# Optimization experiments

Hardware: AMD Instinct MI355X
Metric: run time of the kernel (lower is better)

## Reference

```python
import jax, jax.numpy as jnp
import numpy as np

N_NODES = 131072
N_EDGES = 2097152
B = 256
NODES_PER_GRAPH = 512  # uniform graphs -> to_dense_batch == reshape
F_IN = 74
D = 128
L = 3
EPS = 1e-5


def setup_inputs() -> dict:
    key = jax.random.key(0)
    ks = jax.random.split(key, 12)
    x = jax.random.normal(ks[0], (N_NODES, F_IN), dtype=jnp.float32)
    edge_index = jax.random.randint(ks[1], (2, N_EDGES), 0, N_NODES, dtype=jnp.int32)
    batch = (jnp.arange(N_NODES, dtype=jnp.int32) // NODES_PER_GRAPH)
    s = 1.0 / np.sqrt(D)
    W_init = jax.random.uniform(ks[2], (F_IN, D), jnp.float32, -s, s)
    W_gcn = jax.random.uniform(ks[3], (L, D, D), jnp.float32, -s, s)
    b_gcn = jnp.zeros((L, D), jnp.float32)
    gamma = jnp.ones((L, D), jnp.float32)
    beta = jnp.zeros((L, D), jnp.float32)
    W_res = jax.random.uniform(ks[4], (L, D, D), jnp.float32, -s, s)
    b_res = jax.random.uniform(ks[5], (L, D), jnp.float32, -s, s)
    return {"x": x, "edge_index": edge_index, "batch": batch, "W_init": W_init,
            "W_gcn": W_gcn, "b_gcn": b_gcn, "gamma": gamma, "beta": beta,
            "W_res": W_res, "b_res": b_res}


def _gcn_conv(x, src, tgt, norm, W, b):
    # PyG GCNConv: h = x @ W ; out[tgt] += norm * h[src] ; + bias
    h = x @ W                                    # [N, D]
    msg = h[src] * norm[:, None]                 # [E+N, D] gather (memory-bound)
    out = jax.ops.segment_sum(msg, tgt, num_segments=N_NODES)
    return out + b


def _batchnorm(x, g, bta):
    mean = jnp.mean(x, axis=0)
    var = jnp.var(x, axis=0)  # biased, matches torch BN training forward
    return (x - mean) * jax.lax.rsqrt(var + EPS) * g + bta


def reference(x, edge_index, batch, W_init, W_gcn, b_gcn, gamma, beta, W_res, b_res):
    # add self loops once; symmetric deg^{-1/2} normalization (PyG default)
    loops = jnp.arange(N_NODES, dtype=edge_index.dtype)
    src = jnp.concatenate([edge_index[0], loops])
    tgt = jnp.concatenate([edge_index[1], loops])
    deg = jax.ops.segment_sum(jnp.ones_like(src, dtype=jnp.float32), tgt,
                              num_segments=N_NODES)
    dinv = jnp.where(deg > 0, jax.lax.rsqrt(jnp.maximum(deg, 1.0)), 0.0)
    norm = dinv[src] * dinv[tgt]

    h = x @ W_init                               # init_transform (no bias)
    for i in range(L):
        conv = _gcn_conv(h, src, tgt, norm, W_gcn[i], b_gcn[i])
        h_new = jax.nn.relu(_batchnorm(conv, gamma[i], beta[i]))
        h = h_new + (h @ W_res[i] + b_res[i])
    # to_dense_batch with uniform NODES_PER_GRAPH -> reshape, all mask=True
    return h.reshape(B, NODES_PER_GRAPH, D)
```

## Files before the change

kernel.cpp:

```cpp
#include <hip/hip_runtime.h>

#define NN 131072
#define NE 2097152
#define DD 128
#define LL 3

#define NB 256
#define BSH 9
#define TILE (NE / NB)

typedef __attribute__((ext_vector_type(8))) short short8;
typedef __attribute__((ext_vector_type(4))) float f32x4;

__device__ __forceinline__ ushort f2bf(float f) {
    uint u = __float_as_uint(f);
    return (ushort)((u + 0x7fffu + ((u >> 16) & 1u)) >> 16);
}
__device__ __forceinline__ float bflo(uint u) { return __uint_as_float(u << 16); }
__device__ __forceinline__ float bfhi(uint u) { return __uint_as_float(u & 0xffff0000u); }

__global__ __launch_bounds__(256) void k_prep(const float* __restrict__ x,
                                              const float* __restrict__ Wi,
                                              const float* __restrict__ Wg,
                                              const float* __restrict__ Wr,
                                              uint* __restrict__ xb,
                                              ushort* __restrict__ wt,
                                              float* __restrict__ bns) {
    const int t = threadIdx.x, blk = blockIdx.x;
    const size_t id = (size_t)blk * 256 + t;
    const int n = (int)(id >> 6);
    const int k0 = (int)(id & 63) * 2;
    float v0 = (k0 < 74) ? x[(size_t)n * 74 + k0] : 0.0f;
    float v1 = (k0 + 1 < 74) ? x[(size_t)n * 74 + k0 + 1] : 0.0f;
    xb[id] = (uint)f2bf(v0) | ((uint)f2bf(v1) << 16);
    if (blk < 448) {
        const int id2 = blk * 256 + t;
        const int m = id2 >> 14;
        const int c = (id2 >> 7) & 127;
        const int k = id2 & 127;
        float v;
        if (m == 0)      v = (k < 74) ? Wi[k * DD + c] : 0.0f;
        else if (m <= 3) v = Wg[(size_t)(m - 1) * DD * DD + k * DD + c];
        else             v = Wr[(size_t)(m - 4) * DD * DD + k * DD + c];
        wt[id2] = f2bf(v);
    }
    if (blk == 448) {
        bns[t] = 0.0f; bns[t + 256] = 0.0f; bns[t + 512] = 0.0f;
    }
}

__global__ __launch_bounds__(256) void kA_count(const int* __restrict__ tgt,
                                                int* __restrict__ blockHist) {
    __shared__ int hist[NB];
    const int t = threadIdx.x, blk = blockIdx.x;
    hist[t] = 0;
    __syncthreads();
    const int base = blk * TILE;
#pragma unroll 8
    for (int j = 0; j < TILE / 256; ++j)
        atomicAdd(&hist[tgt[base + j * 256 + t] >> BSH], 1);
    __syncthreads();
    blockHist[t * NB + blk] = hist[t];
}

__global__ __launch_bounds__(256) void kA_scan1(int* __restrict__ blockHist,
                                                int* __restrict__ rowSum) {
    __shared__ int sc[256];
    const int t = threadIdx.x, b = blockIdx.x;
    const int v = blockHist[b * NB + t];
    sc[t] = v;
    __syncthreads();
    for (int off = 1; off < 256; off <<= 1) {
        int a = sc[t];
        int u = (t >= off) ? sc[t - off] : 0;
        __syncthreads();
        sc[t] = a + u;
        __syncthreads();
    }
    blockHist[b * NB + t] = sc[t] - v;
    if (t == 255) rowSum[b] = sc[255];
}

__global__ __launch_bounds__(256) void kA_scan2(const int* __restrict__ rowSum,
                                                int* __restrict__ bstart) {
    __shared__ int sc[256];
    const int t = threadIdx.x;
    const int v = rowSum[t];
    sc[t] = v;
    __syncthreads();
    for (int off = 1; off < 256; off <<= 1) {
        int a = sc[t];
        int u = (t >= off) ? sc[t - off] : 0;
        __syncthreads();
        sc[t] = a + u;
        __syncthreads();
    }
    bstart[t] = sc[t] - v;
    if (t == 255) bstart[NB] = sc[255];
}

__global__ __launch_bounds__(256) void kA_scatter(const int* __restrict__ src,
                                                  const int* __restrict__ tgt,
                                                  const int* __restrict__ chunkBase,
                                                  const int* __restrict__ bstart,
                                                  uint* __restrict__ packed) {
    __shared__ int cur[NB];
    const int t = threadIdx.x, blk = blockIdx.x;
    cur[t] = bstart[t] + chunkBase[t * NB + blk];
    __syncthreads();
    const int base = blk * TILE;
#pragma unroll 4
    for (int j = 0; j < TILE / 256; ++j) {
        const int e = base + j * 256 + t;
        const int tg = tgt[e], s = src[e];
        const int b = tg >> BSH;
        const int pos = atomicAdd(&cur[b], 1);
        packed[pos] = (uint)s | ((uint)(tg & ((1 << BSH) - 1)) << 17);
    }
}

__global__ __launch_bounds__(256) void kB_sort(const uint* __restrict__ packed,
                                               const int* __restrict__ bstart,
                                               int* __restrict__ rowp,
                                               float* __restrict__ dinv,
                                               int* __restrict__ deg,
                                               int* __restrict__ ssrc) {
    __shared__ int cnt[1 << BSH];
    __shared__ int pscan[256];
    const int t = threadIdx.x, b = blockIdx.x;
    const int e0 = bstart[b], e1 = bstart[b + 1];
    cnt[t] = 0; cnt[t + 256] = 0;
    __syncthreads();
    for (int e = e0 + t; e < e1; e += 256)
        atomicAdd(&cnt[packed[e] >> 17], 1);
    __syncthreads();
    const int c0 = cnt[2 * t], c1 = cnt[2 * t + 1];
    pscan[t] = c0 + c1;
    __syncthreads();
    for (int off = 1; off < 256; off <<= 1) {
        int v = pscan[t];
        int u = (t >= off) ? pscan[t - off] : 0;
        __syncthreads();
        pscan[t] = v + u;
        __syncthreads();
    }
    const int ex0 = pscan[t] - c0 - c1;
    const int ex1 = ex0 + c0;
    const int n0 = (b << BSH) + 2 * t;
    rowp[n0] = e0 + ex0;
    rowp[n0 + 1] = e0 + ex1;
    dinv[n0] = rsqrtf((float)(c0 + 1));
    dinv[n0 + 1] = rsqrtf((float)(c1 + 1));
    deg[n0] = c0 + 1;
    deg[n0 + 1] = c1 + 1;
    if (b == NB - 1 && t == 255) rowp[NN] = e1;
    __syncthreads();
    cnt[2 * t] = ex0;
    cnt[2 * t + 1] = ex1;
    __syncthreads();
    for (int e = e0 + t; e < e1; e += 256) {
        const uint p = packed[e];
        const int tl = p >> 17;
        const int pos = atomicAdd(&cnt[tl], 1);
        ssrc[e0 + pos] = (int)(p & 0x1FFFFu);
    }
}

__global__ __launch_bounds__(256) void k_pack(int* __restrict__ ssrc,
                                              const int* __restrict__ deg) {
    const int e = blockIdx.x * 256 + threadIdx.x;
    const int s = ssrc[e];
    ssrc[e] = s | (deg[s] << 17);
}

template <int MODE>
__global__ __launch_bounds__(512) void k_mgemm(const ushort* A,
                                               const ushort* __restrict__ Bt,
                                               ushort* outb,
                                               float* __restrict__ outf,
                                               const ushort* __restrict__ convb,
                                               const float* __restrict__ gamma,
                                               const float* __restrict__ beta,
                                               const float* __restrict__ bres,
                                               float* __restrict__ bnsums) {
    __shared__ ushort As[16384];
    __shared__ ushort Bs[16384];
    __shared__ float sred[256];
    const int t = threadIdx.x;
    const int w = t >> 6, l = t & 63;
    const int lc = l & 15, lr = l >> 4;
    const size_t row0 = (size_t)blockIdx.x * 128;

    for (int ch = w * 4; ch < w * 4 + 4; ++ch) {
        const int row = ch * 4 + lr;
        const int kb = (lc * 16) ^ ((row & 7) << 4);
        const ushort* srcA = A + (row0 + row) * DD + (kb >> 1);
        const ushort* srcB = Bt + (size_t)row * DD + (kb >> 1);
        __builtin_amdgcn_global_load_lds(
            (const __attribute__((address_space(1))) void*)srcA,
            (__attribute__((address_space(3))) void*)(As + ch * 512), 16, 0, 0);
        __builtin_amdgcn_global_load_lds(
            (const __attribute__((address_space(1))) void*)srcB,
            (__attribute__((address_space(3))) void*)(Bs + ch * 512), 16, 0, 0);
    }
    if (MODE == 1 && t < 256) sred[t] = 0.0f;
    if (MODE >= 2 && t < DD) {
        const float invN = 1.0f / (float)NN;
        const float mean = bnsums[t] * invN;
        const float var = bnsums[DD + t] * invN - mean * mean;
        const float sc = gamma[t] * rsqrtf(var + 1e-5f);
        sred[t] = sc;
        sred[DD + t] = beta[t] - mean * sc;
    }
    __syncthreads();

    f32x4 acc[8] = {};
    const char* Ab = (const char*)As;
    const char* Bb = (const char*)Bs;
#pragma unroll
    for (int kk = 0; kk < 4; ++kk) {
        const int kb = kk * 64 + lr * 16;
        const int r = w * 16 + lc;
        const short8 a = *(const short8*)(Ab + r * 256 + (kb ^ ((r & 7) << 4)));
#pragma unroll
        for (int n = 0; n < 8; ++n) {
            const int c = n * 16 + lc;
            short8 b = *(const short8*)(Bb + c * 256 + (kb ^ ((c & 7) << 4)));
            acc[n] = __builtin_amdgcn_mfma_f32_16x16x32_bf16(a, b, acc[n], 0, 0, 0);
        }
    }

    if (MODE == 0) {
#pragma unroll
        for (int n = 0; n < 8; ++n) {
            const int c = n * 16 + lc;
#pragma unroll
            for (int j = 0; j < 4; ++j) {
                const size_t r = row0 + w * 16 + lr * 4 + j;
                outb[r * DD + c] = f2bf(acc[n][j]);
            }
        }
    } else if (MODE == 1) {
#pragma unroll
        for (int n = 0; n < 8; ++n) {
            const int c = n * 16 + lc;
            float ps = 0.0f, ps2 = 0.0f;
#pragma unroll
            for (int j = 0; j < 4; ++j) {
                const size_t r = row0 + w * 16 + lr * 4 + j;
                const float v = acc[n][j];
                outb[r * DD + c] = f2bf(v);
                ps += v; ps2 += v * v;
            }
            atomicAdd(&sred[c], ps);
            atomicAdd(&sred[DD + c], ps2);
        }
        __syncthreads();
        if (t < 256) atomicAdd(&bnsums[t], sred[t]);
    } else {
        float scv[8], shv[8], bbv[8];
#pragma unroll
        for (int n = 0; n < 8; ++n) {
            const int c = n * 16 + lc;
            scv[n] = sred[c]; shv[n] = sred[DD + c]; bbv[n] = bres[c];
        }
#pragma unroll
        for (int n = 0; n < 8; ++n) {
            const int c = n * 16 + lc;
#pragma unroll
            for (int j = 0; j < 4; ++j) {
                const size_t r = row0 + w * 16 + lr * 4 + j;
                const float cv = __uint_as_float((uint)convb[r * DD + c] << 16);
                const float v = fmaxf(cv * scv[n] + shv[n], 0.0f) + acc[n][j] + bbv[n];
                if (MODE == 2) outb[r * DD + c] = f2bf(v);
                if (MODE == 3) outf[r * DD + c] = v;
            }
        }
    }
}

__global__ __launch_bounds__(256) void k_aggregate(const int* __restrict__ rowp,
                                                   const float* __restrict__ dinv,
                                                   const int* __restrict__ ssrc,
                                                   const uint* __restrict__ hb,
                                                   uint* __restrict__ aggb) {
    __shared__ float2 eb[4][64];
    const int wv = threadIdx.x >> 6;
    const int n = blockIdx.x * 4 + wv;
    const int l = threadIdx.x & 63;
    const float dn = dinv[n];
    const uint u0 = hb[((uint)n << 6) + l];
    const float dn2 = dn * dn;
    float ax = dn2 * bflo(u0), ay = dn2 * bfhi(u0);
    const int e0 = rowp[n], e1 = rowp[n + 1];
    for (int base = e0; base < e1; base += 64) {
        const int cnt = min(64, e1 - base);
        float nm = 0.0f; uint sb = 0;
        if (l < cnt) {
            const uint p = (uint)ssrc[base + l];
            sb = (p & 0x1FFFFu) << 6;
            nm = dn * rsqrtf((float)(p >> 17));
        }
        eb[wv][l] = make_float2(nm, __uint_as_float(sb));
        int i = 0;
        for (; i + 16 <= cnt; i += 16) {
            uint vv[16]; float nmv[16];
#pragma unroll
            for (int j = 0; j < 16; ++j) {
                const float2 e = eb[wv][i + j];
                nmv[j] = e.x;
                vv[j] = hb[__float_as_uint(e.y) + l];
            }
#pragma unroll
            for (int j = 0; j < 16; ++j) {
                ax += nmv[j] * bflo(vv[j]);
                ay += nmv[j] * bfhi(vv[j]);
            }
        }
        for (; i < cnt; i += 8) {
            uint vv[8]; float nmv[8];
#pragma unroll
            for (int j = 0; j < 8; ++j) {
                const float2 e = eb[wv][i + j];
                nmv[j] = e.x;
                vv[j] = hb[__float_as_uint(e.y) + l];
            }
#pragma unroll
            for (int j = 0; j < 8; ++j) {
                ax += nmv[j] * bflo(vv[j]);
                ay += nmv[j] * bfhi(vv[j]);
            }
        }
    }
    aggb[((uint)n << 6) + l] = (uint)f2bf(ax) | ((uint)f2bf(ay) << 16);
}

extern "C" void kernel_launch(void* const* d_in, const int* in_sizes, int n_in,
                              void* d_out, int out_size, void* d_ws, size_t ws_size,
                              hipStream_t stream) {
    const float* x      = (const float*)d_in[0];
    const int*   ei     = (const int*)d_in[1];
    const float* W_init = (const float*)d_in[3];
    const float* W_gcn  = (const float*)d_in[4];
    const float* gamma  = (const float*)d_in[6];
    const float* beta   = (const float*)d_in[7];
    const float* W_res  = (const float*)d_in[8];
    const float* b_res  = (const float*)d_in[9];

    float* h = (float*)d_out;
    char* p = (char*)d_ws;
    ushort* aggb = (ushort*)p;           p += (size_t)NN * DD * 2;
    ushort* hb   = (ushort*)p;           p += (size_t)NN * DD * 2;
    ushort* convb = (ushort*)p;          p += (size_t)NN * DD * 2;
    uint*   xb   = (uint*)convb;
    float*  dinv = (float*)p;            p += (size_t)NN * 4;
    int*    deg  = (int*)p;              p += (size_t)NN * 4;
    float*  bns  = (float*)p;            p += 768 * 4;
    ushort* wt   = (ushort*)p;           p += 7 * 16384 * 2;
    int* blockHist = (int*)p;            p += (size_t)NB * NB * 4;
    int* rowSum  = (int*)p;              p += NB * 4;
    int* bstart  = (int*)p;              p += (NB + 1) * 4 + 4;
    uint* packed = (uint*)p;             p += (size_t)NE * 4;
    int* rowp    = (int*)p;              p += ((size_t)NN + 1) * 4 + 4;
    int* ssrc    = (int*)p;

    const int* srcp = ei;
    const int* tgtp = ei + NE;

    k_prep<<<NN * 64 / 256, 256, 0, stream>>>(x, W_init, W_gcn, W_res, xb, wt, bns);
    kA_count<<<NB, 256, 0, stream>>>(tgtp, blockHist);
    kA_scan1<<<NB, 256, 0, stream>>>(blockHist, rowSum);
    kA_scan2<<<1, 256, 0, stream>>>(rowSum, bstart);
    kA_scatter<<<NB, 256, 0, stream>>>(srcp, tgtp, blockHist, bstart, packed);
    kB_sort<<<NB, 256, 0, stream>>>(packed, bstart, rowp, dinv, deg, ssrc);
    k_pack<<<NE / 256, 256, 0, stream>>>(ssrc, deg);

    k_mgemm<0><<<NN / 128, 512, 0, stream>>>((const ushort*)xb, wt, hb,
                                             nullptr, nullptr, nullptr, nullptr,
                                             nullptr, nullptr);

    for (int i = 0; i < LL; ++i) {
        k_aggregate<<<NN / 4, 256, 0, stream>>>(rowp, dinv, ssrc,
                                                (const uint*)hb, (uint*)aggb);
        k_mgemm<1><<<NN / 128, 512, 0, stream>>>(aggb, wt + (size_t)(1 + i) * 16384,
                                                 convb, nullptr, nullptr, nullptr,
                                                 nullptr, nullptr, bns + i * 256);
        if (i < LL - 1)
            k_mgemm<2><<<NN / 128, 512, 0, stream>>>(hb, wt + (size_t)(4 + i) * 16384,
                                                     hb, nullptr, convb,
                                                     gamma + i * DD, beta + i * DD,
                                                     b_res + i * DD, bns + i * 256);
        else
            k_mgemm<3><<<NN / 128, 512, 0, stream>>>(hb, wt + (size_t)(4 + i) * 16384,
                                                     nullptr, h, convb,
                                                     gamma + i * DD, beta + i * DD,
                                                     b_res + i * DD, bns + i * 256);
    }
}
```

Baseline: 550.8 us.

## Double-buffer A tiles in GEMM, reuse weights across four tiles, fuse scan

The MFMA GEMM kernel now has each 256-thread block handle 256 rows as four 64-row tiles. It stages the weight matrix into LDS once per block and double-buffers the A tiles, so the async load of the next tile overlaps compute on the current one. BN partial sums are kept in registers and reduced once per block. The single-block second scan is folded into the scatter kernel, removing one launch at the cost of every block redoing a 256-element scan. Aggregation now uses nontemporal loads for the sorted edge stream. The risks are fewer blocks and waves for the GEMM, and the in-place hb update now relying on row-disjoint aliasing with a restrict-qualified A pointer.

```diff
diff --git a/kernel.cpp b/kernel.cpp
--- a/kernel.cpp
+++ b/kernel.cpp
@@ -81,10 +81,15 @@
     if (t == 255) rowSum[b] = sc[255];
 }
 
-__global__ __launch_bounds__(256) void kA_scan2(const int* __restrict__ rowSum,
-                                                int* __restrict__ bstart) {
+__global__ __launch_bounds__(256) void kA_scatter(const int* __restrict__ src,
+                                                  const int* __restrict__ tgt,
+                                                  const int* __restrict__ chunkBase,
+                                                  const int* __restrict__ rowSum,
+                                                  int* __restrict__ bstart,
+                                                  uint* __restrict__ packed) {
+    __shared__ int cur[NB];
     __shared__ int sc[256];
-    const int t = threadIdx.x;
+    const int t = threadIdx.x, blk = blockIdx.x;
     const int v = rowSum[t];
     sc[t] = v;
     __syncthreads();
@@ -95,18 +100,12 @@
         sc[t] = a + u;
         __syncthreads();
     }
-    bstart[t] = sc[t] - v;
-    if (t == 255) bstart[NB] = sc[255];
-}
-
-__global__ __launch_bounds__(256) void kA_scatter(const int* __restrict__ src,
-                                                  const int* __restrict__ tgt,
-                                                  const int* __restrict__ chunkBase,
-                                                  const int* __restrict__ bstart,
-                                                  uint* __restrict__ packed) {
-    __shared__ int cur[NB];
-    const int t = threadIdx.x, blk = blockIdx.x;
-    cur[t] = bstart[t] + chunkBase[t * NB + blk];
+    const int bst = sc[t] - v;
+    cur[t] = bst + chunkBase[t * NB + blk];
+    if (blk == 0) {
+        bstart[t] = bst;
+        if (t == 255) bstart[NB] = sc[255];
+    }
     __syncthreads();
     const int base = blk * TILE;
 #pragma unroll 4
@@ -173,8 +172,19 @@
     ssrc[e] = s | (deg[s] << 17);
 }
 
+#define STAGE_A(buf, rowbase)                                                  \
+    for (int ch = w * 4; ch < w * 4 + 4; ++ch) {                               \
+        const int row_ = ch * 4 + lr;                                          \
+        const int kb_ = (lc * 16) ^ ((row_ & 7) << 4);                         \
+        const ushort* srcA_ = A + ((rowbase) + row_) * DD + (kb_ >> 1);        \
+        __builtin_amdgcn_global_load_lds(                                      \
+            (const __attribute__((address_space(1))) void*)srcA_,              \
+            (__attribute__((address_space(3))) void*)(As[buf] + ch * 512),     \
+            16, 0, 0);                                                         \
+    }
+
 template <int MODE>
-__global__ __launch_bounds__(512) void k_mgemm(const ushort* A,
+__global__ __launch_bounds__(256) void k_mgemm(const ushort* __restrict__ A,
                                                const ushort* __restrict__ Bt,
                                                ushort* outb,
                                                float* __restrict__ outf,
@@ -183,27 +193,23 @@
                                                const float* __restrict__ beta,
                                                const float* __restrict__ bres,
                                                float* __restrict__ bnsums) {
-    __shared__ ushort As[16384];
     __shared__ ushort Bs[16384];
+    __shared__ ushort As[2][8192];
     __shared__ float sred[256];
     const int t = threadIdx.x;
     const int w = t >> 6, l = t & 63;
     const int lc = l & 15, lr = l >> 4;
-    const size_t row0 = (size_t)blockIdx.x * 128;
-
-    for (int ch = w * 4; ch < w * 4 + 4; ++ch) {
+    const size_t base0 = (size_t)blockIdx.x * 256;
+
+    for (int ch = w * 8; ch < w * 8 + 8; ++ch) {
         const int row = ch * 4 + lr;
         const int kb = (lc * 16) ^ ((row & 7) << 4);
-        const ushort* srcA = A + (row0 + row) * DD + (kb >> 1);
         const ushort* srcB = Bt + (size_t)row * DD + (kb >> 1);
-        __builtin_amdgcn_global_load_lds(
-            (const __attribute__((address_space(1))) void*)srcA,
-            (__attribute__((address_space(3))) void*)(As + ch * 512), 16, 0, 0);
         __builtin_amdgcn_global_load_lds(
             (const __attribute__((address_space(1))) void*)srcB,
             (__attribute__((address_space(3))) void*)(Bs + ch * 512), 16, 0, 0);
     }
-    if (MODE == 1 && t < 256) sred[t] = 0.0f;
+    STAGE_A(0, base0);
     if (MODE >= 2 && t < DD) {
         const float invN = 1.0f / (float)NN;
         const float mean = bnsums[t] * invN;
@@ -214,68 +220,88 @@
     }
     __syncthreads();
 
-    f32x4 acc[8] = {};
-    const char* Ab = (const char*)As;
-    const char* Bb = (const char*)Bs;
-#pragma unroll
-    for (int kk = 0; kk < 4; ++kk) {
-        const int kb = kk * 64 + lr * 16;
-        const int r = w * 16 + lc;
-        const short8 a = *(const short8*)(Ab + r * 256 + (kb ^ ((r & 7) << 4)));
-#pragma unroll
-        for (int n = 0; n < 8; ++n) {
-            const int c = n * 16 + lc;
-            short8 b = *(const short8*)(Bb + c * 256 + (kb ^ ((c & 7) << 4)));
-            acc[n] = __builtin_amdgcn_mfma_f32_16x16x32_bf16(a, b, acc[n], 0, 0, 0);
-        }
-    }
-
-    if (MODE == 0) {
-#pragma unroll
-        for (int n = 0; n < 8; ++n) {
-            const int c = n * 16 + lc;
-#pragma unroll
-            for (int j = 0; j < 4; ++j) {
-                const size_t r = row0 + w * 16 + lr * 4 + j;
-                outb[r * DD + c] = f2bf(acc[n][j]);
-            }
-        }
-    } else if (MODE == 1) {
-#pragma unroll
-        for (int n = 0; n < 8; ++n) {
-            const int c = n * 16 + lc;
-            float ps = 0.0f, ps2 = 0.0f;
-#pragma unroll
-            for (int j = 0; j < 4; ++j) {
-                const size_t r = row0 + w * 16 + lr * 4 + j;
-                const float v = acc[n][j];
-                outb[r * DD + c] = f2bf(v);
-                ps += v; ps2 += v * v;
-            }
-            atomicAdd(&sred[c], ps);
-            atomicAdd(&sred[DD + c], ps2);
-        }
-        __syncthreads();
-        if (t < 256) atomicAdd(&bnsums[t], sred[t]);
-    } else {
-        float scv[8], shv[8], bbv[8];
+    float scv[8], shv[8], bbv[8];
+    if (MODE >= 2) {
 #pragma unroll
         for (int n = 0; n < 8; ++n) {
             const int c = n * 16 + lc;
             scv[n] = sred[c]; shv[n] = sred[DD + c]; bbv[n] = bres[c];
         }
+    }
+    float ps[8] = {}, ps2[8] = {};
+
+    int cur = 0;
+    for (int tt = 0; tt < 4; ++tt) {
+        const size_t row0 = base0 + tt * 64;
+        if (tt < 3) STAGE_A(cur ^ 1, row0 + 64);
+
+        f32x4 acc[8] = {};
+        const char* Ab = (const char*)As[cur];
+        const char* Bb = (const char*)Bs;
+#pragma unroll
+        for (int kk = 0; kk < 4; ++kk) {
+            const int kb = kk * 64 + lr * 16;
+            const int r = w * 16 + lc;
+            const short8 a = *(const short8*)(Ab + r * 256 + (kb ^ ((r & 7) << 4)));
+#pragma unroll
+            for (int n = 0; n < 8; ++n) {
+                const int c = n * 16 + lc;
+                short8 b = *(const short8*)(Bb + c * 256 + (kb ^ ((c & 7) << 4)));
+                acc[n] = __builtin_amdgcn_mfma_f32_16x16x32_bf16(a, b, acc[n], 0, 0, 0);
+            }
+        }
+
+        if (MODE == 0) {
+#pragma unroll
+            for (int n = 0; n < 8; ++n) {
+                const int c = n * 16 + lc;
+#pragma unroll
+                for (int j = 0; j < 4; ++j) {
+                    const size_t r = row0 + w * 16 + lr * 4 + j;
+                    outb[r * DD + c] = f2bf(acc[n][j]);
+                }
+            }
+        } else if (MODE == 1) {
+#pragma unroll
+            for (int n = 0; n < 8; ++n) {
+                const int c = n * 16 + lc;
+#pragma unroll
+                for (int j = 0; j < 4; ++j) {
+                    const size_t r = row0 + w * 16 + lr * 4 + j;
+                    const float v = acc[n][j];
+                    outb[r * DD + c] = f2bf(v);
+                    ps[n] += v; ps2[n] += v * v;
+                }
+            }
+        } else {
+#pragma unroll
+            for (int n = 0; n < 8; ++n) {
+                const int c = n * 16 + lc;
+#pragma unroll
+                for (int j = 0; j < 4; ++j) {
+                    const size_t r = row0 + w * 16 + lr * 4 + j;
+                    const float cv = __uint_as_float((uint)convb[r * DD + c] << 16);
+                    const float v = fmaxf(cv * scv[n] + shv[n], 0.0f) + acc[n][j] + bbv[n];
+                    if (MODE == 2) outb[r * DD + c] = f2bf(v);
+                    if (MODE == 3) outf[r * DD + c] = v;
+                }
+            }
+        }
+        __syncthreads();
+        cur ^= 1;
+    }
+
+    if (MODE == 1) {
+        sred[t] = 0.0f;
+        __syncthreads();
 #pragma unroll
         for (int n = 0; n < 8; ++n) {
             const int c = n * 16 + lc;
-#pragma unroll
-            for (int j = 0; j < 4; ++j) {
-                const size_t r = row0 + w * 16 + lr * 4 + j;
-                const float cv = __uint_as_float((uint)convb[r * DD + c] << 16);
-                const float v = fmaxf(cv * scv[n] + shv[n], 0.0f) + acc[n][j] + bbv[n];
-                if (MODE == 2) outb[r * DD + c] = f2bf(v);
-                if (MODE == 3) outf[r * DD + c] = v;
-            }
-        }
+            atomicAdd(&sred[c], ps[n]);
+            atomicAdd(&sred[DD + c], ps2[n]);
+        }
+        __syncthreads();
+        atomicAdd(&bnsums[t], sred[t]);
     }
 }
 
@@ -297,7 +323,7 @@
         const int cnt = min(64, e1 - base);
         float nm = 0.0f; uint sb = 0;
         if (l < cnt) {
-            const uint p = (uint)ssrc[base + l];
+            const uint p = (uint)__builtin_nontemporal_load(ssrc + base + l);
             sb = (p & 0x1FFFFu) << 6;
             nm = dn * rsqrtf((float)(p >> 17));
         }
@@ -370,28 +396,27 @@
     k_prep<<<NN * 64 / 256, 256, 0, stream>>>(x, W_init, W_gcn, W_res, xb, wt, bns);
     kA_count<<<NB, 256, 0, stream>>>(tgtp, blockHist);
     kA_scan1<<<NB, 256, 0, stream>>>(blockHist, rowSum);
-    kA_scan2<<<1, 256, 0, stream>>>(rowSum, bstart);
-    kA_scatter<<<NB, 256, 0, stream>>>(srcp, tgtp, blockHist, bstart, packed);
+    kA_scatter<<<NB, 256, 0, stream>>>(srcp, tgtp, blockHist, rowSum, bstart, packed);
     kB_sort<<<NB, 256, 0, stream>>>(packed, bstart, rowp, dinv, deg, ssrc);
     k_pack<<<NE / 256, 256, 0, stream>>>(ssrc, deg);
 
-    k_mgemm<0><<<NN / 128, 512, 0, stream>>>((const ushort*)xb, wt, hb,
+    k_mgemm<0><<<NN / 256, 256, 0, stream>>>((const ushort*)xb, wt, hb,
                                              nullptr, nullptr, nullptr, nullptr,
                                              nullptr, nullptr);
 
     for (int i = 0; i < LL; ++i) {
         k_aggregate<<<NN / 4, 256, 0, stream>>>(rowp, dinv, ssrc,
                                                 (const uint*)hb, (uint*)aggb);
-        k_mgemm<1><<<NN / 128, 512, 0, stream>>>(aggb, wt + (size_t)(1 + i) * 16384,
+        k_mgemm<1><<<NN / 256, 256, 0, stream>>>(aggb, wt + (size_t)(1 + i) * 16384,
                                                  convb, nullptr, nullptr, nullptr,
                                                  nullptr, nullptr, bns + i * 256);
         if (i < LL - 1)
-            k_mgemm<2><<<NN / 128, 512, 0, stream>>>(hb, wt + (size_t)(4 + i) * 16384,
+            k_mgemm<2><<<NN / 256, 256, 0, stream>>>(hb, wt + (size_t)(4 + i) * 16384,
                                                      hb, nullptr, convb,
                                                      gamma + i * DD, beta + i * DD,
                                                      b_res + i * DD, bns + i * 256);
         else
-            k_mgemm<3><<<NN / 128, 512, 0, stream>>>(hb, wt + (size_t)(4 + i) * 16384,
+            k_mgemm<3><<<NN / 256, 256, 0, stream>>>(hb, wt + (size_t)(4 + i) * 16384,
                                                      nullptr, h, convb,
                                                      gamma + i * DD, beta + i * DD,
                                                      b_res + i * DD, bns + i * 256);
```

Result: faster. 471.7 us, median of 2 (-14.4%).
